# Kernel optimization log

Measured on AMD Instinct MI355X. Metric: run time of the kernel, lower is better.

## Reference

```python
import jax, jax.numpy as jnp
import numpy as np

UNITS = 2048
INPUT_DIM = 2048
BATCH = 8192


def setup_inputs() -> dict:
    key = jax.random.key(0)
    k_x, k_w = jax.random.split(key)
    inputs = jax.random.normal(k_x, (BATCH, INPUT_DIM), dtype=jnp.float32)
    # random_normal initializer in keras defaults to stddev=0.05
    w = jax.random.normal(k_w, (INPUT_DIM, UNITS), dtype=jnp.float32) * 0.05
    b = jnp.zeros((UNITS,), dtype=jnp.float32)
    return {"inputs": inputs, "w": w, "b": b}


def reference(inputs, w, b):
    # matmul + bias
    result = jnp.matmul(inputs, w) + b  # [B, units]
    # per-row: if first element > 0.5, add 1 to whole row, else subtract 1
    cond = result[:, :1] > 0.5  # [B, 1], broadcasts over row
    return jnp.where(cond, result + 1.0, result - 1.0)
```

## Files before the change

### kernel.cpp

```cpp
#include <hip/hip_runtime.h>
#include <hip/hip_bf16.h>
#include <stdint.h>

#define M_DIM 8192
#define N_DIM 2048
#define K_DIM 2048

typedef __attribute__((ext_vector_type(8))) short bf16x8;
typedef __attribute__((ext_vector_type(8))) short short8;
typedef __attribute__((ext_vector_type(4))) float f32x4;

static __device__ __forceinline__ unsigned short f2bf(float f) {
  union { float f; unsigned u; } a; a.f = f;
  unsigned u = a.u;
  u += 0x7FFFu + ((u >> 16) & 1u);
  return (unsigned short)(u >> 16);
}

static __device__ __forceinline__ void async16(void* lds, const void* g) {
  __builtin_amdgcn_global_load_lds(
      (const __attribute__((address_space(1))) unsigned int*)g,
      (__attribute__((address_space(3))) unsigned int*)lds, 16, 0, 0);
}

#define BAR()                                \
  do {                                       \
    asm volatile("" ::: "memory");           \
    __builtin_amdgcn_s_barrier();            \
    asm volatile("" ::: "memory");           \
  } while (0)
#define VMCNT(n) asm volatile("s_waitcnt vmcnt(" #n ")" ::: "memory")
#define LGK()                                                \
  do {                                                       \
    asm volatile("s_waitcnt lgkmcnt(0)" ::: "memory");       \
    __builtin_amdgcn_sched_barrier(0);                       \
  } while (0)

__global__ __launch_bounds__(256) void k_transW(const float* __restrict__ W,
                                                unsigned short* __restrict__ Wt,
                                                float* __restrict__ wcol) {
  __shared__ float tile[64][65];
  const int bx = blockIdx.x & 31;
  const int by = blockIdx.x >> 5;
  const int n0 = bx * 64, k0 = by * 64;
  const int t = threadIdx.x;
  #pragma unroll
  for (int i = 0; i < 16; ++i) {
    int lin = i * 256 + t;
    int r = lin >> 6, c = lin & 63;
    float v = W[(size_t)(k0 + r) * N_DIM + n0 + c];
    tile[r][c] = v;
    if (bx == 0 && c == 0) wcol[k0 + r] = v;
  }
  __syncthreads();
  #pragma unroll
  for (int i = 0; i < 16; ++i) {
    int lin = i * 256 + t;
    int r = lin >> 6, c = lin & 63;
    Wt[(size_t)(n0 + r) * K_DIM + k0 + c] = f2bf(tile[c][r]);
  }
}

__global__ __launch_bounds__(256) void k_convX(const float* __restrict__ X,
    const float* __restrict__ wcol, const float* __restrict__ b,
    unsigned short* __restrict__ Xb, float* __restrict__ adj) {
  const int m = blockIdx.x;
  const int t = threadIdx.x;
  const float4* xr = (const float4*)(X + (size_t)m * K_DIM);
  const float4* wc = (const float4*)wcol;
  float4 x0 = xr[2 * t], x1 = xr[2 * t + 1];
  float4 w0 = wc[2 * t], w1 = wc[2 * t + 1];
  short8 o;
  o[0] = (short)f2bf(x0.x); o[1] = (short)f2bf(x0.y);
  o[2] = (short)f2bf(x0.z); o[3] = (short)f2bf(x0.w);
  o[4] = (short)f2bf(x1.x); o[5] = (short)f2bf(x1.y);
  o[6] = (short)f2bf(x1.z); o[7] = (short)f2bf(x1.w);
  *(short8*)(Xb + (size_t)m * K_DIM + t * 8) = o;
  double s = (double)x0.x * w0.x + (double)x0.y * w0.y +
             (double)x0.z * w0.z + (double)x0.w * w0.w +
             (double)x1.x * w1.x + (double)x1.y * w1.y +
             (double)x1.z * w1.z + (double)x1.w * w1.w;
  #pragma unroll
  for (int off = 32; off > 0; off >>= 1) s += __shfl_down(s, off, 64);
  __shared__ double red[4];
  if ((t & 63) == 0) red[t >> 6] = s;
  __syncthreads();
  if (t == 0) {
    double tot = red[0] + red[1] + red[2] + red[3] + (double)b[0];
    adj[m] = (tot > 0.5) ? 1.0f : -1.0f;
  }
}

__device__ __forceinline__ void stage_unit(char* ldsc,
    const unsigned short* __restrict__ src, int row0, int kt,
    int isB, int sel, int wid, int l) {
  char* base = ldsc + (size_t)(kt & 1) * 65536 + (size_t)isB * 32768;
  #pragma unroll
  for (int j = 0; j < 2; ++j) {
    int s = wid * 2 + j;
    int sub_c = s & 1;
    int idx = s >> 1;
    int sub_r = isB ? ((idx & 1) + (idx >> 1) * 4 + sel * 2)
                    : ((idx & 3) + ((idx & 4) ? 8 : 0) + sel * 4);
    int grow = row0 + sub_r * 16 + (l >> 2);
    int gcol = kt * 64 + sub_c * 32 + (((l & 3) * 8) ^ ((l & 32) >> 1));
    async16(base + (size_t)(sub_r * 2 + sub_c) * 1024,
            src + (size_t)grow * K_DIM + gcol);
  }
}

__global__ __launch_bounds__(512, 1) void k_gemm8(
    const unsigned short* __restrict__ A,
    const unsigned short* __restrict__ B,
    const float* __restrict__ bias,
    const float* __restrict__ adj,
    float* __restrict__ out) {
  __shared__ unsigned short lds[2 * 2 * 256 * 64];
  char* ldsc = (char*)lds;

  const int t = threadIdx.x;
  const int wid = t >> 6, l = t & 63;
  const int wm = wid >> 2, wn = wid & 3;

  const int bid = blockIdx.x;
  const int swz = (bid & 7) * 32 + (bid >> 3);
  const int bm = swz >> 3, bn = swz & 7;
  const int m0 = bm * 256, n0 = bn * 256;

  const int r = l & 15, q = l >> 4;
  const int rdoff = (r * 64 + q * 16) ^ ((r & 8) << 2);

  const char* ab0 = ldsc;
  const char* bb0 = ldsc + 32768;
  const char* ab1 = ldsc + 65536;
  const char* bb1 = ldsc + 98304;

  f32x4 acc[8][4] = {};
  bf16x8 af0[2][4], af1[2][4], bv0[2][2], bv1[2][2];

#define STG(isB, sel, kt) \
  stage_unit(ldsc, (isB) ? B : A, (isB) ? n0 : m0, kt, isB, sel, wid, l)

#define RD_A(DST, MH, AB)                                                   \
  _Pragma("unroll") for (int mi4 = 0; mi4 < 4; ++mi4) {                     \
    const int sub_r = wm * 8 + (MH) * 4 + mi4;                              \
    _Pragma("unroll") for (int ks = 0; ks < 2; ++ks)                        \
      DST[ks][mi4] =                                                        \
          *(const bf16x8*)((AB) + (size_t)(sub_r * 2 + ks) * 1024 + rdoff); \
  }

#define RD_B(DST, NH, BB)                                                   \
  _Pragma("unroll") for (int ni2 = 0; ni2 < 2; ++ni2) {                     \
    const int sub_r = wn * 4 + (NH) * 2 + ni2;                              \
    _Pragma("unroll") for (int ks = 0; ks < 2; ++ks)                        \
      DST[ks][ni2] =                                                        \
          *(const bf16x8*)((BB) + (size_t)(sub_r * 2 + ks) * 1024 + rdoff); \
  }

#define CL(MH, NH, AF, BV)                                                  \
  __builtin_amdgcn_s_setprio(1);                                            \
  _Pragma("unroll") for (int ks = 0; ks < 2; ++ks)                          \
    _Pragma("unroll") for (int mi4 = 0; mi4 < 4; ++mi4)                     \
      _Pragma("unroll") for (int ni2 = 0; ni2 < 2; ++ni2)                   \
        acc[(MH) * 4 + mi4][(NH) * 2 + ni2] =                               \
            __builtin_amdgcn_mfma_f32_16x16x32_bf16(                        \
                AF[ks][mi4], BV[ks][ni2],                                   \
                acc[(MH) * 4 + mi4][(NH) * 2 + ni2], 0, 0, 0);              \
  __builtin_amdgcn_s_setprio(0);

#define PH(RD_STMT, STG_STMT, CL_STMT, WAIT_STMT)                           \
  {                                                                         \
    RD_STMT;                                                                \
    STG_STMT;                                                               \
    BAR();                                                                  \
    LGK();                                                                  \
    CL_STMT;                                                                \
    WAIT_STMT;                                                              \
    BAR();                                                                  \
  }

  STG(0, 0, 0); STG(1, 0, 0); STG(1, 1, 0); STG(0, 1, 0);
  STG(0, 0, 1); STG(1, 0, 1);
  VMCNT(4);
  BAR();

  for (int i = 0; i < 15; ++i) {
    const int t1 = 2 * i + 1, t2 = 2 * i + 2, t3 = 2 * i + 3;
    PH(RD_A(af0, 0, ab0); RD_B(bv0, 0, bb0), STG(1, 1, t1),
       CL(0, 0, af0, bv0), );
    PH(RD_B(bv1, 1, bb0), STG(0, 1, t1), CL(0, 1, af0, bv1), );
    PH(RD_A(af1, 1, ab0), STG(0, 0, t2), CL(1, 0, af1, bv0), );
    PH(, STG(1, 0, t2), CL(1, 1, af1, bv1), VMCNT(4));
    PH(RD_A(af0, 0, ab1); RD_B(bv0, 0, bb1), STG(1, 1, t2),
       CL(0, 0, af0, bv0), );
    PH(RD_B(bv1, 1, bb1), STG(0, 1, t2), CL(0, 1, af0, bv1), );
    PH(RD_A(af1, 1, ab1), STG(0, 0, t3), CL(1, 0, af1, bv0), );
    PH(, STG(1, 0, t3), CL(1, 1, af1, bv1), VMCNT(4));
  }
  PH(RD_A(af0, 0, ab0); RD_B(bv0, 0, bb0), STG(1, 1, 31),
     CL(0, 0, af0, bv0), );
  PH(RD_B(bv1, 1, bb0), STG(0, 1, 31), CL(0, 1, af0, bv1), );
  PH(RD_A(af1, 1, ab0), , CL(1, 0, af1, bv0), );
  PH(, , CL(1, 1, af1, bv1), VMCNT(0));
  PH(RD_A(af0, 0, ab1); RD_B(bv0, 0, bb1), , CL(0, 0, af0, bv0), );
  PH(RD_B(bv1, 1, bb1), , CL(0, 1, af0, bv1), );
  PH(RD_A(af1, 1, ab1), , CL(1, 0, af1, bv0), );
  PH(, , CL(1, 1, af1, bv1), );

#undef PH
#undef CL
#undef RD_A
#undef RD_B
#undef STG

  #pragma unroll
  for (int mi = 0; mi < 8; ++mi) {
    const int rowb = m0 + wm * 128 + mi * 16 + q * 4;
    float adjv[4];
    #pragma unroll
    for (int j = 0; j < 4; ++j) adjv[j] = adj[rowb + j];
    #pragma unroll
    for (int ni = 0; ni < 4; ++ni) {
      const int col = n0 + wn * 64 + ni * 16 + r;
      const float bvs = bias[col];
      #pragma unroll
      for (int j = 0; j < 4; ++j)
        out[(size_t)(rowb + j) * N_DIM + col] = acc[mi][ni][j] + bvs + adjv[j];
    }
  }
}

__global__ __launch_bounds__(256) void k_gemm_f32(const float* __restrict__ X,
    const float* __restrict__ W, const float* __restrict__ b,
    float* __restrict__ out) {
  __shared__ float As[16][16];
  __shared__ float Bs[16][17];
  const int bn = blockIdx.x & 127, bm = blockIdx.x >> 7;
  const int tx = threadIdx.x & 15, ty = threadIdx.x >> 4;
  const int row = bm * 16 + ty, col = bn * 16 + tx;
  float acc = 0.f;
  for (int k0 = 0; k0 < K_DIM; k0 += 16) {
    As[ty][tx] = X[(size_t)row * K_DIM + k0 + tx];
    Bs[ty][tx] = W[(size_t)(k0 + ty) * N_DIM + col];
    __syncthreads();
    #pragma unroll
    for (int kk = 0; kk < 16; ++kk) acc += As[ty][kk] * Bs[kk][tx];
    __syncthreads();
  }
  out[(size_t)row * N_DIM + col] = acc + b[col];
}

__global__ __launch_bounds__(256) void k_rowadj(float* __restrict__ out) {
  const int m = blockIdx.x;
  const float c0 = out[(size_t)m * N_DIM];
  __syncthreads();
  const float a = (c0 > 0.5f) ? 1.0f : -1.0f;
  for (int n = threadIdx.x; n < N_DIM; n += 256)
    out[(size_t)m * N_DIM + n] += a;
}

extern "C" void kernel_launch(void* const* d_in, const int* in_sizes, int n_in,
                              void* d_out, int out_size, void* d_ws, size_t ws_size,
                              hipStream_t stream) {
  const float* X = (const float*)d_in[0];
  const float* W = (const float*)d_in[1];
  const float* b = (const float*)d_in[2];
  float* out = (float*)d_out;

  const size_t XB_OFF   = 0;
  const size_t WT_OFF   = (size_t)M_DIM * K_DIM * 2;
  const size_t ADJ_OFF  = WT_OFF + (size_t)N_DIM * K_DIM * 2;
  const size_t WCOL_OFF = ADJ_OFF + (size_t)M_DIM * 4;
  const size_t NEED     = WCOL_OFF + (size_t)K_DIM * 4;

  if (ws_size >= NEED) {
    unsigned short* Xb  = (unsigned short*)((char*)d_ws + XB_OFF);
    unsigned short* Wt  = (unsigned short*)((char*)d_ws + WT_OFF);
    float* adj  = (float*)((char*)d_ws + ADJ_OFF);
    float* wcol = (float*)((char*)d_ws + WCOL_OFF);
    k_transW<<<dim3(1024), dim3(256), 0, stream>>>(W, Wt, wcol);
    k_convX<<<dim3(M_DIM), dim3(256), 0, stream>>>(X, wcol, b, Xb, adj);
    k_gemm8<<<dim3((M_DIM / 256) * (N_DIM / 256)), dim3(512), 0, stream>>>(
        Xb, Wt, b, adj, out);
  } else {
    k_gemm_f32<<<dim3((M_DIM / 16) * (N_DIM / 16)), dim3(256), 0, stream>>>(
        X, W, b, out);
    k_rowadj<<<dim3(M_DIM), dim3(256), 0, stream>>>(out);
  }
}
```

Baseline: 91.14 us.

## Merge W transpose and X conversion into one prep kernel; overlap epilogue stores

Merges the W transpose/convert kernel and the X convert plus row-sign kernel into a single launch whose block index picks the job. The row-sign dot product now reads the first column of W straight from global memory, removing the wcol staging buffer and the dependency between the two kernels. The GEMM epilogue preloads bias and adj into registers and writes each output quarter right after its last MFMA block, so stores overlap the remaining compute. The strided W column reads in the X blocks are uncoalesced and repeated for every row.

```diff
diff --git a/kernel.cpp b/kernel.cpp
--- a/kernel.cpp
+++ b/kernel.cpp
@@ -36,58 +36,53 @@
     __builtin_amdgcn_sched_barrier(0);                       \
   } while (0)
 
-__global__ __launch_bounds__(256) void k_transW(const float* __restrict__ W,
-                                                unsigned short* __restrict__ Wt,
-                                                float* __restrict__ wcol) {
+__global__ __launch_bounds__(256) void k_prep(const float* __restrict__ W,
+    const float* __restrict__ X, const float* __restrict__ b,
+    unsigned short* __restrict__ Wt, unsigned short* __restrict__ Xb,
+    float* __restrict__ adj) {
   __shared__ float tile[64][65];
-  const int bx = blockIdx.x & 31;
-  const int by = blockIdx.x >> 5;
-  const int n0 = bx * 64, k0 = by * 64;
   const int t = threadIdx.x;
-  #pragma unroll
-  for (int i = 0; i < 16; ++i) {
-    int lin = i * 256 + t;
-    int r = lin >> 6, c = lin & 63;
-    float v = W[(size_t)(k0 + r) * N_DIM + n0 + c];
-    tile[r][c] = v;
-    if (bx == 0 && c == 0) wcol[k0 + r] = v;
-  }
-  __syncthreads();
-  #pragma unroll
-  for (int i = 0; i < 16; ++i) {
-    int lin = i * 256 + t;
-    int r = lin >> 6, c = lin & 63;
-    Wt[(size_t)(n0 + r) * K_DIM + k0 + c] = f2bf(tile[c][r]);
-  }
-}
-
-__global__ __launch_bounds__(256) void k_convX(const float* __restrict__ X,
-    const float* __restrict__ wcol, const float* __restrict__ b,
-    unsigned short* __restrict__ Xb, float* __restrict__ adj) {
-  const int m = blockIdx.x;
-  const int t = threadIdx.x;
-  const float4* xr = (const float4*)(X + (size_t)m * K_DIM);
-  const float4* wc = (const float4*)wcol;
-  float4 x0 = xr[2 * t], x1 = xr[2 * t + 1];
-  float4 w0 = wc[2 * t], w1 = wc[2 * t + 1];
-  short8 o;
-  o[0] = (short)f2bf(x0.x); o[1] = (short)f2bf(x0.y);
-  o[2] = (short)f2bf(x0.z); o[3] = (short)f2bf(x0.w);
-  o[4] = (short)f2bf(x1.x); o[5] = (short)f2bf(x1.y);
-  o[6] = (short)f2bf(x1.z); o[7] = (short)f2bf(x1.w);
-  *(short8*)(Xb + (size_t)m * K_DIM + t * 8) = o;
-  double s = (double)x0.x * w0.x + (double)x0.y * w0.y +
-             (double)x0.z * w0.z + (double)x0.w * w0.w +
-             (double)x1.x * w1.x + (double)x1.y * w1.y +
-             (double)x1.z * w1.z + (double)x1.w * w1.w;
-  #pragma unroll
-  for (int off = 32; off > 0; off >>= 1) s += __shfl_down(s, off, 64);
-  __shared__ double red[4];
-  if ((t & 63) == 0) red[t >> 6] = s;
-  __syncthreads();
-  if (t == 0) {
-    double tot = red[0] + red[1] + red[2] + red[3] + (double)b[0];
-    adj[m] = (tot > 0.5) ? 1.0f : -1.0f;
+  if (blockIdx.x < 1024) {
+    const int bx = blockIdx.x & 31;
+    const int by = blockIdx.x >> 5;
+    const int n0 = bx * 64, k0 = by * 64;
+    #pragma unroll
+    for (int i = 0; i < 16; ++i) {
+      int lin = i * 256 + t;
+      int rr = lin >> 6, c = lin & 63;
+      tile[rr][c] = W[(size_t)(k0 + rr) * N_DIM + n0 + c];
+    }
+    __syncthreads();
+    #pragma unroll
+    for (int i = 0; i < 16; ++i) {
+      int lin = i * 256 + t;
+      int rr = lin >> 6, c = lin & 63;
+      Wt[(size_t)(n0 + rr) * K_DIM + k0 + c] = f2bf(tile[c][rr]);
+    }
+  } else {
+    const int m = blockIdx.x - 1024;
+    const float4* xr = (const float4*)(X + (size_t)m * K_DIM);
+    float4 x0 = xr[2 * t], x1 = xr[2 * t + 1];
+    short8 o;
+    o[0] = (short)f2bf(x0.x); o[1] = (short)f2bf(x0.y);
+    o[2] = (short)f2bf(x0.z); o[3] = (short)f2bf(x0.w);
+    o[4] = (short)f2bf(x1.x); o[5] = (short)f2bf(x1.y);
+    o[6] = (short)f2bf(x1.z); o[7] = (short)f2bf(x1.w);
+    *(short8*)(Xb + (size_t)m * K_DIM + t * 8) = o;
+    double s = 0.0;
+    const float xv[8] = {x0.x, x0.y, x0.z, x0.w, x1.x, x1.y, x1.z, x1.w};
+    #pragma unroll
+    for (int i = 0; i < 8; ++i)
+      s += (double)xv[i] * (double)W[(size_t)(t * 8 + i) * N_DIM];
+    #pragma unroll
+    for (int off = 32; off > 0; off >>= 1) s += __shfl_down(s, off, 64);
+    __shared__ double red[4];
+    if ((t & 63) == 0) red[t >> 6] = s;
+    __syncthreads();
+    if (t == 0) {
+      double tot = red[0] + red[1] + red[2] + red[3] + (double)b[0];
+      adj[m] = (tot > 0.5) ? 1.0f : -1.0f;
+    }
   }
 }
 
@@ -168,6 +163,17 @@
                 acc[(MH) * 4 + mi4][(NH) * 2 + ni2], 0, 0, 0);              \
   __builtin_amdgcn_s_setprio(0);
 
+#define STQ(MH, NH)                                                         \
+  _Pragma("unroll") for (int mi4 = 0; mi4 < 4; ++mi4)                       \
+    _Pragma("unroll") for (int ni2 = 0; ni2 < 2; ++ni2) {                   \
+      const int mi = (MH) * 4 + mi4, ni = (NH) * 2 + ni2;                   \
+      const int col = n0 + wn * 64 + ni * 16 + r;                           \
+      const int rowb = m0 + wm * 128 + mi * 16 + q * 4;                     \
+      _Pragma("unroll") for (int j = 0; j < 4; ++j)                         \
+        out[(size_t)(rowb + j) * N_DIM + col] =                             \
+            acc[mi][ni][j] + bias_r[ni] + adj_r[mi][j];                     \
+    }
+
 #define PH(RD_STMT, STG_STMT, CL_STMT, WAIT_STMT)                           \
   {                                                                         \
     RD_STMT;                                                                \
@@ -202,32 +208,31 @@
   PH(RD_B(bv1, 1, bb0), STG(0, 1, 31), CL(0, 1, af0, bv1), );
   PH(RD_A(af1, 1, ab0), , CL(1, 0, af1, bv0), );
   PH(, , CL(1, 1, af1, bv1), VMCNT(0));
-  PH(RD_A(af0, 0, ab1); RD_B(bv0, 0, bb1), , CL(0, 0, af0, bv0), );
-  PH(RD_B(bv1, 1, bb1), , CL(0, 1, af0, bv1), );
-  PH(RD_A(af1, 1, ab1), , CL(1, 0, af1, bv0), );
-  PH(, , CL(1, 1, af1, bv1), );
+
+  float4 adj_r[8];
+  float bias_r[4];
+  #pragma unroll
+  for (int mi = 0; mi < 8; ++mi)
+    adj_r[mi] = *(const float4*)&adj[m0 + wm * 128 + mi * 16 + q * 4];
+  #pragma unroll
+  for (int ni = 0; ni < 4; ++ni)
+    bias_r[ni] = bias[n0 + wn * 64 + ni * 16 + r];
+
+  PH(RD_A(af0, 0, ab1); RD_B(bv0, 0, bb1), , CL(0, 0, af0, bv0); STQ(0, 0), );
+  PH(RD_B(bv1, 1, bb1), , CL(0, 1, af0, bv1); STQ(0, 1), );
+  PH(RD_A(af1, 1, ab1), , CL(1, 0, af1, bv0); STQ(1, 0), );
+  {
+    LGK();
+    CL(1, 1, af1, bv1);
+    STQ(1, 1);
+  }
 
 #undef PH
+#undef STQ
 #undef CL
 #undef RD_A
 #undef RD_B
 #undef STG
-
-  #pragma unroll
-  for (int mi = 0; mi < 8; ++mi) {
-    const int rowb = m0 + wm * 128 + mi * 16 + q * 4;
-    float adjv[4];
-    #pragma unroll
-    for (int j = 0; j < 4; ++j) adjv[j] = adj[rowb + j];
-    #pragma unroll
-    for (int ni = 0; ni < 4; ++ni) {
-      const int col = n0 + wn * 64 + ni * 16 + r;
-      const float bvs = bias[col];
-      #pragma unroll
-      for (int j = 0; j < 4; ++j)
-        out[(size_t)(rowb + j) * N_DIM + col] = acc[mi][ni][j] + bvs + adjv[j];
-    }
-  }
 }
 
 __global__ __launch_bounds__(256) void k_gemm_f32(const float* __restrict__ X,
@@ -270,16 +275,13 @@
   const size_t XB_OFF   = 0;
   const size_t WT_OFF   = (size_t)M_DIM * K_DIM * 2;
   const size_t ADJ_OFF  = WT_OFF + (size_t)N_DIM * K_DIM * 2;
-  const size_t WCOL_OFF = ADJ_OFF + (size_t)M_DIM * 4;
-  const size_t NEED     = WCOL_OFF + (size_t)K_DIM * 4;
+  const size_t NEED     = ADJ_OFF + (size_t)M_DIM * 4;
 
   if (ws_size >= NEED) {
     unsigned short* Xb  = (unsigned short*)((char*)d_ws + XB_OFF);
     unsigned short* Wt  = (unsigned short*)((char*)d_ws + WT_OFF);
     float* adj  = (float*)((char*)d_ws + ADJ_OFF);
-    float* wcol = (float*)((char*)d_ws + WCOL_OFF);
-    k_transW<<<dim3(1024), dim3(256), 0, stream>>>(W, Wt, wcol);
-    k_convX<<<dim3(M_DIM), dim3(256), 0, stream>>>(X, wcol, b, Xb, adj);
+    k_prep<<<dim3(1024 + M_DIM), dim3(256), 0, stream>>>(W, X, b, Wt, Xb, adj);
     k_gemm8<<<dim3((M_DIM / 256) * (N_DIM / 256)), dim3(512), 0, stream>>>(
         Xb, Wt, b, adj, out);
   } else {
```

After: 138.9 us. +52.4%, slower.
